# Kernel optimization log

Measured on AMD Instinct MI355X. Metric: run time of the kernel, lower is better.

The kernel has to match this reference:

```python
import jax, jax.numpy as jnp
import numpy as np

B = 16          # number of point clouds in batch (points.batch.max()+1)
C = 256         # feature channels
N = 65536       # total points across batch
LIDAR_POINTS = 32768
NUM_UPSAMPLE_UNIT = 2
L = LIDAR_POINTS // (2 ** NUM_UPSAMPLE_UNIT)  # 8192, output length per sample


def setup_inputs() -> dict:
    key = jax.random.key(0)
    k1, k2, k3 = jax.random.split(key, 3)
    points_x = jax.random.normal(k1, (N, 3), dtype=jnp.float32)
    point_features = jax.random.normal(k2, (N, C), dtype=jnp.float32)
    # per-point batch id, sorted (torch_geometric convention)
    batch = jnp.sort(jax.random.randint(k3, (N,), 0, B)).astype(jnp.int32)
    return {"points_x": points_x, "point_features": point_features, "batch": batch}


def reference(points_x, point_features, batch):
    # Per-batch counts and start offsets (points are sorted by batch id).
    counts = jax.ops.segment_sum(jnp.ones((N,), jnp.int32), batch, num_segments=B)  # [B]
    offsets = jnp.concatenate([jnp.zeros((1,), jnp.int32), jnp.cumsum(counts)[:-1]])  # [B]
    # torch nn.Upsample(scale_factor=r, mode='nearest') with r = L/n maps
    # output index j -> input index floor(j / r) = floor(j * n / L).
    j = jnp.arange(L, dtype=jnp.int32)                      # [L]
    src = offsets[:, None] + (j[None, :] * counts[:, None]) // L  # [B, L] global gather indices
    out_feature = point_features[src].transpose(0, 2, 1)    # [B, C, L]
    out_point = points_x[src, :3].transpose(0, 2, 1)        # [B, 3, L]
    return (out_point, out_feature)
```

## Files before the change

### kernel.cpp

```cpp
#include <hip/hip_runtime.h>

#define NPTS     65536
#define BATCHES  16
#define CHANNELS 256
#define LOUT     8192
#define TJ       128
#define MAX_ROWS 72
#define STRIDE   257

__global__ void k_offsets(const int* __restrict__ batch, int* __restrict__ ws) {
    const int t = threadIdx.x;
    __shared__ int bnd[BATCHES + 1];
    if (t <= BATCHES) {
        int lo = 0;
        if (t == BATCHES) {
            lo = NPTS;
        } else {
            int hi = NPTS;
            while (lo < hi) {
                int mid = (lo + hi) >> 1;
                if (batch[mid] < t) lo = mid + 1; else hi = mid;
            }
        }
        bnd[t] = lo;
    }
    __syncthreads();
    if (t < BATCHES) {
        ws[t]           = bnd[t];
        ws[BATCHES + t] = bnd[t + 1] - bnd[t];
    }
}

__global__ __launch_bounds__(256, 2) void k_main(
    const float* __restrict__ px,
    const float* __restrict__ pf,
    const int*   __restrict__ ws,
    float*       __restrict__ out)
{
    __shared__ float tile[MAX_ROWS * STRIDE];
    const int t    = threadIdx.x;
    const int lane = t & 63;
    const int wv   = t >> 6;
    const int b    = blockIdx.x >> 6;
    const int j0   = (blockIdx.x & 63) * TJ;
    const int offs = ws[b];
    const int cnt  = ws[BATCHES + b];

    auto srow = [&](int j) -> int {
        int s = offs + ((j * cnt) >> 13);
        return s < (NPTS - 1) ? s : (NPTS - 1);
    };

    const int s0 = srow(j0);
    const int s1 = srow(j0 + TJ - 1);
    const int R  = s1 - s0 + 1;

    const int j  = j0 + lane * 2;
    const int ga = srow(j);
    const int gb = srow(j + 1);

    float* outf = out + (size_t)BATCHES * 3 * LOUT;

    if (R <= MAX_ROWS) {
        const float4* in4 = (const float4*)(pf + (size_t)s0 * CHANNELS);
        const int n4 = R * (CHANNELS / 4);
        for (int e = t; e < n4; e += 256) {
            const int row = e >> 6;
            const int c4  = e & 63;
            const float4 v = in4[row * 64 + c4];
            float* dst = &tile[row * STRIDE + c4 * 4];
            dst[0] = v.x; dst[1] = v.y; dst[2] = v.z; dst[3] = v.w;
        }
        __syncthreads();

        const int la = (ga - s0) * STRIDE;
        const int lb = (gb - s0) * STRIDE;
        float* op = outf + ((size_t)b * CHANNELS) * LOUT + j;
        #pragma unroll 4
        for (int c = wv; c < CHANNELS; c += 4) {
            float2 v;
            v.x = tile[la + c];
            v.y = tile[lb + c];
            *(float2*)(op + (size_t)c * LOUT) = v;
        }
    } else {
        const float* ra = pf + (size_t)ga * CHANNELS;
        const float* rb = pf + (size_t)gb * CHANNELS;
        float* op = outf + ((size_t)b * CHANNELS) * LOUT + j;
        for (int c = wv; c < CHANNELS; c += 4) {
            float2 v;
            v.x = ra[c];
            v.y = rb[c];
            *(float2*)(op + (size_t)c * LOUT) = v;
        }
    }

    if (wv < 3) {
        const int d = wv;
        float2 v;
        v.x = px[ga * 3 + d];
        v.y = px[gb * 3 + d];
        *(float2*)(out + ((size_t)(b * 3 + d)) * LOUT + j) = v;
    }
}

extern "C" void kernel_launch(void* const* d_in, const int* in_sizes, int n_in,
                              void* d_out, int out_size, void* d_ws, size_t ws_size,
                              hipStream_t stream) {
    const float* px    = (const float*)d_in[0];
    const float* pf    = (const float*)d_in[1];
    const int*   batch = (const int*)d_in[2];
    float* out = (float*)d_out;
    int*   wsI = (int*)d_ws;

    k_offsets<<<1, 32, 0, stream>>>(batch, wsI);
    k_main<<<BATCHES * (LOUT / TJ), 256, 0, stream>>>(px, pf, wsI, out);
}
```

Baseline: 209.8 us.

## Fuse offset search into main kernel, halve tile width, use nontemporal stores

Removes the separate single-block offsets kernel: each block now binary-searches its own batch start and end in the sorted batch array, which drops one launch and the dependency between kernels. The output tile shrinks from 128 to 64 columns, so each lane writes one scalar instead of a float2. The block count doubles and the launch bounds allow 4 blocks per CU, since the smaller LDS tile permits it. Output stores become nontemporal to avoid polluting cache, at the cost of narrower per-lane writes and redundant binary searches in every block.

Measured after the change: 200.5 us. 4.4% less time.

```diff
diff --git a/kernel.cpp b/kernel.cpp
--- a/kernel.cpp
+++ b/kernel.cpp
@@ -4,50 +4,46 @@
 #define BATCHES  16
 #define CHANNELS 256
 #define LOUT     8192
-#define TJ       128
-#define MAX_ROWS 72
+#define TJ       64
+#define NTILES   (LOUT / TJ)
+#define MAX_ROWS 38
 #define STRIDE   257
 
-__global__ void k_offsets(const int* __restrict__ batch, int* __restrict__ ws) {
-    const int t = threadIdx.x;
-    __shared__ int bnd[BATCHES + 1];
-    if (t <= BATCHES) {
+__global__ __launch_bounds__(256, 4) void k_main(
+    const float* __restrict__ px,
+    const float* __restrict__ pf,
+    const int*   __restrict__ batch,
+    float*       __restrict__ out)
+{
+    __shared__ float tile[MAX_ROWS * STRIDE];
+    __shared__ int   sb[2];
+
+    const int t    = threadIdx.x;
+    const int lane = t & 63;
+    const int wv   = t >> 6;
+    const int b    = blockIdx.x >> 7;
+    const int j0   = (blockIdx.x & (NTILES - 1)) * TJ;
+
+    if (t < 2) {
+        const int target = b + t;
         int lo = 0;
-        if (t == BATCHES) {
+        if (target >= BATCHES) {
             lo = NPTS;
         } else {
             int hi = NPTS;
             while (lo < hi) {
-                int mid = (lo + hi) >> 1;
-                if (batch[mid] < t) lo = mid + 1; else hi = mid;
+                const int mid = (lo + hi) >> 1;
+                if (batch[mid] < target) lo = mid + 1; else hi = mid;
             }
         }
-        bnd[t] = lo;
+        sb[t] = lo;
     }
     __syncthreads();
-    if (t < BATCHES) {
-        ws[t]           = bnd[t];
-        ws[BATCHES + t] = bnd[t + 1] - bnd[t];
-    }
-}
-
-__global__ __launch_bounds__(256, 2) void k_main(
-    const float* __restrict__ px,
-    const float* __restrict__ pf,
-    const int*   __restrict__ ws,
-    float*       __restrict__ out)
-{
-    __shared__ float tile[MAX_ROWS * STRIDE];
-    const int t    = threadIdx.x;
-    const int lane = t & 63;
-    const int wv   = t >> 6;
-    const int b    = blockIdx.x >> 6;
-    const int j0   = (blockIdx.x & 63) * TJ;
-    const int offs = ws[b];
-    const int cnt  = ws[BATCHES + b];
+    const int offs = sb[0];
+    const int cnt  = sb[1] - sb[0];
 
     auto srow = [&](int j) -> int {
-        int s = offs + ((j * cnt) >> 13);
+        const int s = offs + ((j * cnt) >> 13);
         return s < (NPTS - 1) ? s : (NPTS - 1);
     };
 
@@ -55,9 +51,8 @@
     const int s1 = srow(j0 + TJ - 1);
     const int R  = s1 - s0 + 1;
 
-    const int j  = j0 + lane * 2;
+    const int j  = j0 + lane;
     const int ga = srow(j);
-    const int gb = srow(j + 1);
 
     float* outf = out + (size_t)BATCHES * 3 * LOUT;
 
@@ -74,33 +69,22 @@
         __syncthreads();
 
         const int la = (ga - s0) * STRIDE;
-        const int lb = (gb - s0) * STRIDE;
         float* op = outf + ((size_t)b * CHANNELS) * LOUT + j;
-        #pragma unroll 4
+        #pragma unroll 8
         for (int c = wv; c < CHANNELS; c += 4) {
-            float2 v;
-            v.x = tile[la + c];
-            v.y = tile[lb + c];
-            *(float2*)(op + (size_t)c * LOUT) = v;
+            __builtin_nontemporal_store(tile[la + c], op + (size_t)c * LOUT);
         }
     } else {
         const float* ra = pf + (size_t)ga * CHANNELS;
-        const float* rb = pf + (size_t)gb * CHANNELS;
         float* op = outf + ((size_t)b * CHANNELS) * LOUT + j;
         for (int c = wv; c < CHANNELS; c += 4) {
-            float2 v;
-            v.x = ra[c];
-            v.y = rb[c];
-            *(float2*)(op + (size_t)c * LOUT) = v;
+            __builtin_nontemporal_store(ra[c], op + (size_t)c * LOUT);
         }
     }
 
     if (wv < 3) {
-        const int d = wv;
-        float2 v;
-        v.x = px[ga * 3 + d];
-        v.y = px[gb * 3 + d];
-        *(float2*)(out + ((size_t)(b * 3 + d)) * LOUT + j) = v;
+        __builtin_nontemporal_store(px[ga * 3 + wv],
+                                    out + ((size_t)(b * 3 + wv)) * LOUT + j);
     }
 }
 
@@ -111,8 +95,6 @@
     const float* pf    = (const float*)d_in[1];
     const int*   batch = (const int*)d_in[2];
     float* out = (float*)d_out;
-    int*   wsI = (int*)d_ws;
 
-    k_offsets<<<1, 32, 0, stream>>>(batch, wsI);
-    k_main<<<BATCHES * (LOUT / TJ), 256, 0, stream>>>(px, pf, wsI, out);
+    k_main<<<BATCHES * NTILES, 256, 0, stream>>>(px, pf, batch, out);
 }
```
